# Optimization experiments

Measured on AMD Instinct MI355X. Metric: run time of the kernel, lower is better.

Reference implementation:

```python
import jax, jax.numpy as jnp
import numpy as np

EMBED_DIM = 1024
NUM_HEADS = 16
HEAD_DIM = EMBED_DIM // NUM_HEADS
B, S = 2, 2048
NEG = -1e20


def setup_inputs() -> dict:
    key = jax.random.key(0)
    ks = jax.random.split(key, 8)
    scale = 0.02
    return {
        "query": jax.random.normal(ks[0], (B, S, EMBED_DIM), jnp.float32),
        "keys": jax.random.normal(ks[1], (B, S, EMBED_DIM), jnp.float32),
        "values": jax.random.normal(ks[2], (B, S, EMBED_DIM), jnp.float32),
        "mask": jax.random.randint(ks[3], (1, 1, S, S), 0, 2, jnp.int32),
        "Wq": jax.random.normal(ks[4], (EMBED_DIM, EMBED_DIM), jnp.float32) * scale,
        "Wk": jax.random.normal(ks[5], (EMBED_DIM, EMBED_DIM), jnp.float32) * scale,
        "Wv": jax.random.normal(ks[6], (EMBED_DIM, EMBED_DIM), jnp.float32) * scale,
        "Wo": jax.random.normal(ks[7], (EMBED_DIM, EMBED_DIM), jnp.float32) * scale,
        "bo": jnp.zeros((EMBED_DIM,), jnp.float32),
    }


def reference(query, keys, values, mask, Wq, Wk, Wv, Wo, bo):
    N, Lq, _ = query.shape
    Lk = keys.shape[1]
    # torch nn.Linear: y = x @ W.T  (bias=False for Q/K/V)
    Q = (query @ Wq.T).reshape(N, Lq, NUM_HEADS, HEAD_DIM)
    K = (keys @ Wk.T).reshape(N, Lk, NUM_HEADS, HEAD_DIM)
    V = (values @ Wv.T).reshape(N, Lk, NUM_HEADS, HEAD_DIM)
    # NOTE: source scales by sqrt(embed_dim), not sqrt(head_dim) — kept faithful.
    energy = jnp.einsum("nqhd,nkhd->nhqk", Q, K) / jnp.sqrt(
        jnp.asarray(EMBED_DIM, Q.dtype)
    )
    energy = jnp.where(mask == 0, jnp.asarray(NEG, energy.dtype), energy)
    attention = jax.nn.softmax(energy, axis=3)
    out = jnp.einsum("nhqk,nkhd->nqhd", attention, V).reshape(N, Lq, EMBED_DIM)
    return out @ Wo.T + bo
```

## Files before the change

kernel.cpp:

```cpp
#include <hip/hip_runtime.h>
#include <stdint.h>

typedef __bf16 bf16;
typedef __bf16 bf16x4 __attribute__((ext_vector_type(4)));
typedef __bf16 bf16x8 __attribute__((ext_vector_type(8)));
typedef float f32x4 __attribute__((ext_vector_type(4)));
typedef float f32x16 __attribute__((ext_vector_type(16)));
typedef unsigned int uintx2 __attribute__((ext_vector_type(2)));
typedef unsigned int uintx4 __attribute__((ext_vector_type(4)));

#define MFMA16(a, b, c) __builtin_amdgcn_mfma_f32_16x16x32_bf16((a), (b), (c), 0, 0, 0)
#define MFMA32(a, b, c) __builtin_amdgcn_mfma_f32_32x32x16_bf16((a), (b), (c), 0, 0, 0)

__device__ __forceinline__ void gload16(const bf16* g, bf16* l) {
    __builtin_amdgcn_global_load_lds(
        (const __attribute__((address_space(1))) void*)g,
        (__attribute__((address_space(3))) void*)l, 16, 0, 0);
}

__device__ __forceinline__ float fast_exp2(float x) {
#if __has_builtin(__builtin_amdgcn_exp2f)
    return __builtin_amdgcn_exp2f(x);
#else
    return exp2f(x);
#endif
}

__global__ __launch_bounds__(256) void cvt_kernel(
    const float* __restrict__ q, const float* __restrict__ k, const float* __restrict__ v,
    const float* __restrict__ wq, const float* __restrict__ wk,
    const float* __restrict__ wv, const float* __restrict__ wo,
    const int* __restrict__ mask,
    bf16* __restrict__ qb, bf16* __restrict__ kb, bf16* __restrict__ vb,
    bf16* __restrict__ wqb, bf16* __restrict__ wkb, bf16* __restrict__ wvb,
    bf16* __restrict__ wob, unsigned long long* __restrict__ maskb)
{
    int z = blockIdx.z;
    if (z == 7) {
        int t16 = blockIdx.x * 256 + threadIdx.x;
        if (t16 >= 262144) return;
        const int4* mp = (const int4*)mask + (size_t)t16 * 4;
        unsigned bits = 0;
#pragma unroll
        for (int c = 0; c < 4; ++c) {
            int4 a = mp[c];
            bits |= (unsigned)(a.x != 0) << (c * 4 + 0);
            bits |= (unsigned)(a.y != 0) << (c * 4 + 1);
            bits |= (unsigned)(a.z != 0) << (c * 4 + 2);
            bits |= (unsigned)(a.w != 0) << (c * 4 + 3);
        }
        unsigned long long u = (unsigned long long)bits << (16 * (threadIdx.x & 3));
        u |= __shfl_xor(u, 1, 64);
        u |= __shfl_xor(u, 2, 64);
        if ((threadIdx.x & 3) == 0) maskb[t16 >> 2] = u;
        return;
    }
    const float* src; bf16* dst; int n;
    switch (z) {
        case 0:  src = q;  dst = qb;  n = 4194304; break;
        case 1:  src = k;  dst = kb;  n = 4194304; break;
        case 2:  src = v;  dst = vb;  n = 4194304; break;
        case 3:  src = wq; dst = wqb; n = 1048576; break;
        case 4:  src = wk; dst = wkb; n = 1048576; break;
        case 5:  src = wv; dst = wvb; n = 1048576; break;
        default: src = wo; dst = wob; n = 1048576; break;
    }
    int i = (blockIdx.x * 256 + threadIdx.x) * 8;
    if (i >= n) return;
    float4 f0 = *(const float4*)(src + i);
    float4 f1 = *(const float4*)(src + i + 4);
    bf16x8 o;
    o[0] = (bf16)f0.x; o[1] = (bf16)f0.y; o[2] = (bf16)f0.z; o[3] = (bf16)f0.w;
    o[4] = (bf16)f1.x; o[5] = (bf16)f1.y; o[6] = (bf16)f1.z; o[7] = (bf16)f1.w;
    *(bf16x8*)(dst + i) = o;
}

template <int OUTMODE>
__global__ __launch_bounds__(256) void gemm_kernel(
    const bf16* __restrict__ A0, const bf16* __restrict__ A1, const bf16* __restrict__ A2,
    const bf16* __restrict__ B0, const bf16* __restrict__ B1, const bf16* __restrict__ B2,
    bf16* __restrict__ C0, bf16* __restrict__ C1, bf16* __restrict__ Vt,
    const float* __restrict__ bias, float* __restrict__ outf)
{
    constexpr int TN    = (OUTMODE == 0) ? 128 : 64;
    constexpr int NI    = TN / 32;
    constexpr int BUFSZ = 4096 + TN * 32;
    __shared__ bf16 smem[3 * BUFSZ];

    const int f = blockIdx.x + 8 * blockIdx.y + ((OUTMODE == 0) ? 256 * blockIdx.z : 0);
    const int xcd = f & 7, sidx = f >> 3;
    const int z  = (OUTMODE == 0) ? (sidx >> 5) : 0;
    const int m0 = (xcd * 4 + (sidx & 3)) * 128;
    const int n0 = (OUTMODE == 0) ? ((sidx >> 2) & 7) * 128 : (sidx >> 2) * 64;

    const bf16* A = (z == 0) ? A0 : (z == 1) ? A1 : A2;
    const bf16* B = (z == 0) ? B0 : (z == 1) ? B1 : B2;

    const int tid  = threadIdx.x;
    const int lane = tid & 63;
    const int wave = tid >> 6;
    const int quad = lane >> 4;
    const int l16  = lane & 15;
    const int wm = (wave >> 1) * 64;
    const int wn = (wave & 1) * (TN / 2);

    const int lrow = lane >> 2;
    const int lcol = (lane & 3) * 8;

    f32x4 acc[4][NI] = {};

    const bf16* Ag = A + (size_t)(m0 + lrow) * 1024 + lcol;
    const bf16* Bg = B + (size_t)(n0 + lrow) * 1024 + lcol;

    bf16* buf0 = smem;
    bf16* buf1 = smem + BUFSZ;
    bf16* buf2 = smem + 2 * BUFSZ;

    auto stage = [&](bf16* base, int k0) {
#pragma unroll
        for (int j = 0; j < 2; ++j)
            gload16(Ag + (size_t)(wave * 32 + j * 16) * 1024 + k0,
                    base + (wave * 32 + j * 16) * 32);
        bf16* Btb = base + 4096;
        if constexpr (OUTMODE == 0) {
#pragma unroll
            for (int j = 0; j < 2; ++j)
                gload16(Bg + (size_t)(wave * 32 + j * 16) * 1024 + k0,
                        Btb + (wave * 32 + j * 16) * 32);
        } else {
            gload16(Bg + (size_t)(wave * 16) * 1024 + k0, Btb + (wave * 16) * 32);
        }
    };

    auto step = [&](bf16* cb, bf16* sb, int k0) {
        if (k0 == 992) {
            asm volatile("s_waitcnt vmcnt(0)" ::: "memory");
        } else if constexpr (OUTMODE == 0) {
            asm volatile("s_waitcnt vmcnt(4)" ::: "memory");
        } else {
            asm volatile("s_waitcnt vmcnt(3)" ::: "memory");
        }
        __builtin_amdgcn_s_barrier();
        __builtin_amdgcn_sched_barrier(0);
        if (k0 + 64 < 1024) stage(sb, k0 + 64);

        const bf16* Btb = cb + 4096;
        bf16x8 af[4], bg[NI];
#pragma unroll
        for (int i = 0; i < 4; ++i)
            af[i] = *(const bf16x8*)(cb + (wm + i * 16 + l16) * 32 + quad * 8);
#pragma unroll
        for (int j = 0; j < NI; ++j)
            bg[j] = *(const bf16x8*)(Btb + (wn + j * 16 + l16) * 32 + quad * 8);
#pragma unroll
        for (int i = 0; i < 4; ++i)
#pragma unroll
            for (int j = 0; j < NI; ++j)
                acc[i][j] = MFMA16(af[i], bg[j], acc[i][j]);
    };

    stage(buf0, 0);
    stage(buf1, 32);
    for (int k0 = 0; k0 < 960; k0 += 96) {
        step(buf0, buf2, k0);
        step(buf1, buf0, k0 + 32);
        step(buf2, buf1, k0 + 64);
    }
    step(buf0, buf2, 960);
    step(buf1, buf0, 992);

    if constexpr (OUTMODE == 0) {
        if (z == 2) {
            __syncthreads();
            const int qsw = ((quad & 1) << 1) | (quad >> 1);
#pragma unroll
            for (int i = 0; i < 4; ++i)
#pragma unroll
                for (int j = 0; j < 4; ++j) {
                    int e  = wn + j * 16 + l16;
                    int sp = wm + i * 16 + qsw * 4;
                    bf16x4 v4;
#pragma unroll
                    for (int r = 0; r < 4; ++r) v4[r] = (bf16)acc[i][j][r];
                    *(bf16x4*)(smem + e * 136 + sp) = v4;
                }
            __syncthreads();
            const int bq = m0 >> 11;
            const int srow = m0 & 2047;
#pragma unroll
            for (int c = 0; c < 2; ++c) {
                int idx = c * 256 + tid;
                int e = idx >> 2, sc = (idx & 3) * 32;
                bf16* dst = Vt + (size_t)(bq * 1024 + n0 + e) * 2048 + srow + sc;
#pragma unroll
                for (int kk = 0; kk < 4; ++kk)
                    *(bf16x8*)(dst + kk * 8) =
                        *(const bf16x8*)(smem + e * 136 + sc + kk * 8);
            }
            return;
        }
        bf16* C = (z == 0) ? C0 : C1;
        const float cs = (z == 0) ? 0.0450842200277800f : 1.0f;
#pragma unroll
        for (int i = 0; i < 4; ++i)
#pragma unroll
            for (int j = 0; j < 4; ++j) {
                int row = m0 + wm + i * 16 + quad * 4;
                int col = n0 + wn + j * 16 + l16;
#pragma unroll
                for (int r = 0; r < 4; ++r)
                    C[(row + r) * 1024 + col] = (bf16)(acc[i][j][r] * cs);
            }
    } else {
#pragma unroll
        for (int j = 0; j < NI; ++j) {
            int col = n0 + wn + j * 16 + l16;
            float bj = bias[col];
#pragma unroll
            for (int i = 0; i < 4; ++i) {
                int row = m0 + wm + i * 16 + quad * 4;
#pragma unroll
                for (int r = 0; r < 4; ++r)
                    outf[(row + r) * 1024 + col] = acc[i][j][r] + bj;
            }
        }
    }
}

__global__ __launch_bounds__(512, 4) void flash_kernel(
    const bf16* __restrict__ Q, const bf16* __restrict__ K, const bf16* __restrict__ Vt,
    const unsigned long long* __restrict__ maskb, bf16* __restrict__ O)
{
    __shared__ char smem[65536];

    const int tid  = threadIdx.x;
    const int lane = tid & 63;
    const int wave = tid >> 6;
    const int half = wave >> 2;
    const int w4   = wave & 3;
    const int l32  = lane & 31;
    const int hl   = lane >> 5;
    const int l7   = lane & 7;

    const int flat = blockIdx.x + 16 * (blockIdx.y + 16 * blockIdx.z);
    const int xcd  = flat & 7;
    const int slot = flat >> 3;
    const int bh   = xcd * 4 + (slot >> 4);
    const int h  = bh & 15;
    const int b  = bh >> 4;
    const int q0 = (slot & 15) * 128;
    const int qt = q0 + w4 * 32;

    bf16* hbase = (bf16*)smem + half * 16384;
    bf16* K0 = hbase;
    bf16* K1 = hbase + 4096;
    bf16* V0 = hbase + 8192;
    bf16* V1 = hbase + 12288;

    const bf16* Qb = Q + (size_t)(b * 2048 + qt + l32) * 1024 + h * 64 + hl * 8;
    bf16x8 qf[4];
#pragma unroll
    for (int ks = 0; ks < 4; ++ks) qf[ks] = *(const bf16x8*)(Qb + ks * 16);

    bf16x8 ones;
#pragma unroll
    for (int j = 0; j < 8; ++j) ones[j] = (bf16)1.0f;

    f32x16 acc[2] = {};
    f32x16 lacc = {};

    const int dmarow = lane >> 3;
    const int dmacol = (l7 ^ dmarow) * 8;
    const bf16* Kg = K + (size_t)(b * 2048 + w4 * 16 + dmarow) * 1024 + h * 64 + dmacol;
    const bf16* Vg = Vt + (size_t)((b * 16 + h) * 64 + w4 * 16 + dmarow) * 2048 + dmacol;
    const unsigned long long* Mg = maskb + (size_t)(qt + l32) * 32 + half * 16;
    const int kbase = half * 1024;

    auto stage = [&](bf16* Kd, bf16* Vd, int ktAbs) {
        gload16(Kg + (size_t)ktAbs * 1024,       Kd + (w4 * 16) * 64);
        gload16(Kg + (size_t)(ktAbs + 8) * 1024, Kd + (w4 * 16 + 8) * 64);
        gload16(Vg + ktAbs,                      Vd + (w4 * 16) * 64);
        gload16(Vg + ktAbs + 8 * 2048,           Vd + (w4 * 16 + 8) * 64);
    };

    unsigned long long mw = Mg[0];
    stage(K0, V0, kbase);

    auto body = [&](const bf16* Kc, const bf16* Vc, bf16* Kn, bf16* Vn, int it) {
        __syncthreads();
        unsigned long long mw_next = 0;
        if (it + 1 < 16) {
            stage(Kn, Vn, kbase + (it + 1) * 64);
            mw_next = Mg[it + 1];
        }

        bf16x8 pa[4];
#pragma unroll
        for (int t = 0; t < 2; ++t) {
            f32x16 s = {};
            __builtin_amdgcn_s_setprio(1);
#pragma unroll
            for (int ks = 0; ks < 4; ++ks) {
                bf16x8 ka = *(const bf16x8*)(Kc + (t * 32 + l32) * 64 +
                                             (((ks * 2 + hl) ^ l7) * 8));
                s = MFMA32(ka, qf[ks], s);
            }
            __builtin_amdgcn_s_setprio(0);
            unsigned mwt = (unsigned)(mw >> (t * 32 + 4 * hl));
            unsigned W[4][2];
#pragma unroll
            for (int g = 0; g < 4; ++g) {
                bf16x4 pv;
#pragma unroll
                for (int r = 0; r < 4; ++r) {
                    float ev = fast_exp2(s[g * 4 + r]);
                    unsigned msk = (unsigned)((int)(mwt << (31 - (8 * g + r))) >> 31);
                    unsigned evu = __builtin_bit_cast(unsigned, ev) & msk;
                    pv[r] = (bf16)__builtin_bit_cast(float, evu);
                }
                uintx2 u = __builtin_bit_cast(uintx2, pv);
                W[g][0] = u[0];
                W[g][1] = u[1];
            }
#pragma unroll
            for (int kh = 0; kh < 2; ++kh) {
                uintx4 aw = { W[2 * kh][0], W[2 * kh][1],
                              W[2 * kh + 1][0], W[2 * kh + 1][1] };
                pa[t * 2 + kh] = __builtin_bit_cast(bf16x8, aw);
            }
        }

        __builtin_amdgcn_s_setprio(1);
#pragma unroll
        for (int dt = 0; dt < 2; ++dt)
#pragma unroll
            for (int ks = 0; ks < 4; ++ks) {
                bf16x8 vb = *(const bf16x8*)(Vc + (dt * 32 + l32) * 64 +
                                             (((ks * 2 + hl) ^ l7) * 8));
                acc[dt] = MFMA32(pa[ks], vb, acc[dt]);
            }
#pragma unroll
        for (int ks = 0; ks < 4; ++ks)
            lacc = MFMA32(pa[ks], ones, lacc);
        __builtin_amdgcn_s_setprio(0);

        mw = mw_next;
    };

    for (int it = 0; it < 16; it += 2) {
        body(K0, V0, K1, V1, it);
        body(K1, V1, K0, V0, it + 1);
    }

    __syncthreads();
    float* cb = (float*)smem;
    float* ex = cb + (w4 * 64 + lane) * 4;
    if (half == 1) {
#pragma unroll
        for (int i = 0; i < 4; ++i) {
            f32x4 t0, t1, t2;
#pragma unroll
            for (int j = 0; j < 4; ++j) {
                t0[j] = acc[0][i * 4 + j];
                t1[j] = acc[1][i * 4 + j];
                t2[j] = lacc[i * 4 + j];
            }
            *(f32x4*)(ex + (i + 0) * 1024) = t0;
            *(f32x4*)(ex + (i + 4) * 1024) = t1;
            *(f32x4*)(ex + (i + 8) * 1024) = t2;
        }
    }
    __syncthreads();
    if (half == 0) {
#pragma unroll
        for (int i = 0; i < 4; ++i) {
            f32x4 t0 = *(const f32x4*)(ex + (i + 0) * 1024);
            f32x4 t1 = *(const f32x4*)(ex + (i + 4) * 1024);
            f32x4 t2 = *(const f32x4*)(ex + (i + 8) * 1024);
#pragma unroll
            for (int j = 0; j < 4; ++j) {
                acc[0][i * 4 + j] += t0[j];
                acc[1][i * 4 + j] += t1[j];
                lacc[i * 4 + j]   += t2[j];
            }
        }

        const size_t obase = (size_t)(b * 2048 + qt) * 1024 + h * 64;
#pragma unroll
        for (int g = 0; g < 4; ++g)
#pragma unroll
            for (int r = 0; r < 4; ++r) {
                int qr = 4 * hl + 8 * g + r;
                float inv = 1.0f / lacc[g * 4 + r];
                O[obase + (size_t)qr * 1024 + l32]      = (bf16)(acc[0][g * 4 + r] * inv);
                O[obase + (size_t)qr * 1024 + 32 + l32] = (bf16)(acc[1][g * 4 + r] * inv);
            }
    }
}

extern "C" void kernel_launch(void* const* d_in, const int* in_sizes, int n_in,
                              void* d_out, int out_size, void* d_ws, size_t ws_size,
                              hipStream_t stream)
{
    const float* q  = (const float*)d_in[0];
    const float* k  = (const float*)d_in[1];
    const float* v  = (const float*)d_in[2];
    const int* mask = (const int*)d_in[3];
    const float* wq = (const float*)d_in[4];
    const float* wk = (const float*)d_in[5];
    const float* wv = (const float*)d_in[6];
    const float* wo = (const float*)d_in[7];
    const float* bo = (const float*)d_in[8];
    float* out = (float*)d_out;

    char* p = (char*)d_ws;
    auto alloc = [&](size_t bytes) {
        char* r = p;
        p += (bytes + 255) & ~(size_t)255;
        return r;
    };
    const size_t SB = (size_t)4096 * 1024 * 2;
    const size_t WB = (size_t)1024 * 1024 * 2;
    bf16* qb  = (bf16*)alloc(SB);
    bf16* kb  = (bf16*)alloc(SB);
    bf16* vb  = (bf16*)alloc(SB);
    bf16* wqb = (bf16*)alloc(WB);
    bf16* wkb = (bf16*)alloc(WB);
    bf16* wvb = (bf16*)alloc(WB);
    bf16* wob = (bf16*)alloc(WB);
    bf16* Qp  = (bf16*)alloc(SB);
    bf16* Kp  = (bf16*)alloc(SB);
    bf16* Vtp = (bf16*)alloc(SB);
    bf16* Ob  = (bf16*)alloc(SB);
    unsigned long long* maskb = (unsigned long long*)alloc(2048 * 32 * 8);

    cvt_kernel<<<dim3(2048, 1, 8), 256, 0, stream>>>(
        q, k, v, wq, wk, wv, wo, mask, qb, kb, vb, wqb, wkb, wvb, wob, maskb);

    gemm_kernel<0><<<dim3(8, 32, 3), 256, 0, stream>>>(
        qb, kb, vb, wqb, wkb, wvb, Qp, Kp, Vtp, nullptr, nullptr);

    flash_kernel<<<dim3(16, 16, 2), 512, 0, stream>>>(Qp, Kp, Vtp, maskb, Ob);

    gemm_kernel<1><<<dim3(8, 64, 1), 256, 0, stream>>>(
        Ob, nullptr, nullptr, wob, nullptr, nullptr,
        nullptr, nullptr, nullptr, bo, out);
}
```

Measured before the change: 227.9 us.

## Fuse fp32-to-bf16 conversion of QKV inputs and weights into the projection GEMM

Removes the separate conversion pass over q/k/v and Wq/Wk/Wv. The QKV GEMM now loads fp32 tiles into registers, converts them to bf16, and writes them into a double-buffered LDS tile, using register prefetch in place of the direct global-to-LDS async loads. This avoids writing and re-reading roughly 30 MB of bf16 intermediates. The cost is twice the global read bytes per tile (fp32), repeated conversion work, and a simpler pipeline that may hide latency less well. The prep kernel now converts only Wo and packs the mask.

```diff
diff --git a/kernel.cpp b/kernel.cpp
--- a/kernel.cpp
+++ b/kernel.cpp
@@ -26,75 +26,57 @@
 #endif
 }
 
-__global__ __launch_bounds__(256) void cvt_kernel(
-    const float* __restrict__ q, const float* __restrict__ k, const float* __restrict__ v,
-    const float* __restrict__ wq, const float* __restrict__ wk,
-    const float* __restrict__ wv, const float* __restrict__ wo,
-    const int* __restrict__ mask,
-    bf16* __restrict__ qb, bf16* __restrict__ kb, bf16* __restrict__ vb,
-    bf16* __restrict__ wqb, bf16* __restrict__ wkb, bf16* __restrict__ wvb,
+__global__ __launch_bounds__(256) void prep_kernel(
+    const float* __restrict__ wo, const int* __restrict__ mask,
     bf16* __restrict__ wob, unsigned long long* __restrict__ maskb)
 {
-    int z = blockIdx.z;
-    if (z == 7) {
-        int t16 = blockIdx.x * 256 + threadIdx.x;
-        if (t16 >= 262144) return;
-        const int4* mp = (const int4*)mask + (size_t)t16 * 4;
-        unsigned bits = 0;
-#pragma unroll
-        for (int c = 0; c < 4; ++c) {
-            int4 a = mp[c];
-            bits |= (unsigned)(a.x != 0) << (c * 4 + 0);
-            bits |= (unsigned)(a.y != 0) << (c * 4 + 1);
-            bits |= (unsigned)(a.z != 0) << (c * 4 + 2);
-            bits |= (unsigned)(a.w != 0) << (c * 4 + 3);
-        }
-        unsigned long long u = (unsigned long long)bits << (16 * (threadIdx.x & 3));
-        u |= __shfl_xor(u, 1, 64);
-        u |= __shfl_xor(u, 2, 64);
-        if ((threadIdx.x & 3) == 0) maskb[t16 >> 2] = u;
+    int bid = blockIdx.x;
+    if (bid < 512) {
+        int i = (bid * 256 + threadIdx.x) * 8;
+        float4 f0 = *(const float4*)(wo + i);
+        float4 f1 = *(const float4*)(wo + i + 4);
+        bf16x8 o;
+        o[0] = (bf16)f0.x; o[1] = (bf16)f0.y; o[2] = (bf16)f0.z; o[3] = (bf16)f0.w;
+        o[4] = (bf16)f1.x; o[5] = (bf16)f1.y; o[6] = (bf16)f1.z; o[7] = (bf16)f1.w;
+        *(bf16x8*)(wob + i) = o;
         return;
     }
-    const float* src; bf16* dst; int n;
-    switch (z) {
-        case 0:  src = q;  dst = qb;  n = 4194304; break;
-        case 1:  src = k;  dst = kb;  n = 4194304; break;
-        case 2:  src = v;  dst = vb;  n = 4194304; break;
-        case 3:  src = wq; dst = wqb; n = 1048576; break;
-        case 4:  src = wk; dst = wkb; n = 1048576; break;
-        case 5:  src = wv; dst = wvb; n = 1048576; break;
-        default: src = wo; dst = wob; n = 1048576; break;
-    }
-    int i = (blockIdx.x * 256 + threadIdx.x) * 8;
-    if (i >= n) return;
-    float4 f0 = *(const float4*)(src + i);
-    float4 f1 = *(const float4*)(src + i + 4);
-    bf16x8 o;
-    o[0] = (bf16)f0.x; o[1] = (bf16)f0.y; o[2] = (bf16)f0.z; o[3] = (bf16)f0.w;
-    o[4] = (bf16)f1.x; o[5] = (bf16)f1.y; o[6] = (bf16)f1.z; o[7] = (bf16)f1.w;
-    *(bf16x8*)(dst + i) = o;
-}
-
-template <int OUTMODE>
-__global__ __launch_bounds__(256) void gemm_kernel(
-    const bf16* __restrict__ A0, const bf16* __restrict__ A1, const bf16* __restrict__ A2,
-    const bf16* __restrict__ B0, const bf16* __restrict__ B1, const bf16* __restrict__ B2,
-    bf16* __restrict__ C0, bf16* __restrict__ C1, bf16* __restrict__ Vt,
-    const float* __restrict__ bias, float* __restrict__ outf)
+    int t16 = (bid - 512) * 256 + threadIdx.x;
+    const int4* mp = (const int4*)mask + (size_t)t16 * 4;
+    unsigned bits = 0;
+#pragma unroll
+    for (int c = 0; c < 4; ++c) {
+        int4 a = mp[c];
+        bits |= (unsigned)(a.x != 0) << (c * 4 + 0);
+        bits |= (unsigned)(a.y != 0) << (c * 4 + 1);
+        bits |= (unsigned)(a.z != 0) << (c * 4 + 2);
+        bits |= (unsigned)(a.w != 0) << (c * 4 + 3);
+    }
+    unsigned long long u = (unsigned long long)bits << (16 * (threadIdx.x & 3));
+    u |= __shfl_xor(u, 1, 64);
+    u |= __shfl_xor(u, 2, 64);
+    if ((threadIdx.x & 3) == 0) maskb[t16 >> 2] = u;
+}
+
+__global__ __launch_bounds__(256) void gemm_qkv_kernel(
+    const float* __restrict__ A0, const float* __restrict__ A1, const float* __restrict__ A2,
+    const float* __restrict__ B0, const float* __restrict__ B1, const float* __restrict__ B2,
+    bf16* __restrict__ C0, bf16* __restrict__ C1, bf16* __restrict__ Vt)
 {
-    constexpr int TN    = (OUTMODE == 0) ? 128 : 64;
-    constexpr int NI    = TN / 32;
-    constexpr int BUFSZ = 4096 + TN * 32;
-    __shared__ bf16 smem[3 * BUFSZ];
-
-    const int f = blockIdx.x + 8 * blockIdx.y + ((OUTMODE == 0) ? 256 * blockIdx.z : 0);
+    __shared__ bf16 smem[17408];
+    bf16* A0l = smem;
+    bf16* B0l = smem + 4096;
+    bf16* A1l = smem + 8192;
+    bf16* B1l = smem + 12288;
+
+    const int f = blockIdx.x + 8 * blockIdx.y + 256 * blockIdx.z;
     const int xcd = f & 7, sidx = f >> 3;
-    const int z  = (OUTMODE == 0) ? (sidx >> 5) : 0;
+    const int z  = sidx >> 5;
     const int m0 = (xcd * 4 + (sidx & 3)) * 128;
-    const int n0 = (OUTMODE == 0) ? ((sidx >> 2) & 7) * 128 : (sidx >> 2) * 64;
-
-    const bf16* A = (z == 0) ? A0 : (z == 1) ? A1 : A2;
-    const bf16* B = (z == 0) ? B0 : (z == 1) ? B1 : B2;
+    const int n0 = ((sidx >> 2) & 7) * 128;
+
+    const float* A = (z == 0) ? A0 : (z == 1) ? A1 : A2;
+    const float* B = (z == 0) ? B0 : (z == 1) ? B1 : B2;
 
     const int tid  = threadIdx.x;
     const int lane = tid & 63;
@@ -102,15 +84,144 @@
     const int quad = lane >> 4;
     const int l16  = lane & 15;
     const int wm = (wave >> 1) * 64;
-    const int wn = (wave & 1) * (TN / 2);
+    const int wn = (wave & 1) * 64;
 
     const int lrow = lane >> 2;
     const int lcol = (lane & 3) * 8;
 
-    f32x4 acc[4][NI] = {};
-
-    const bf16* Ag = A + (size_t)(m0 + lrow) * 1024 + lcol;
-    const bf16* Bg = B + (size_t)(n0 + lrow) * 1024 + lcol;
+    f32x4 acc[4][4] = {};
+    float4 ra[2][2], rb[2][2];
+
+    const float* Ag = A + (size_t)(m0 + wave * 32 + lrow) * 1024 + lcol;
+    const float* Bg = B + (size_t)(n0 + wave * 32 + lrow) * 1024 + lcol;
+    const int lds_off = lrow * 32 + lcol;
+
+    auto loadregs = [&](int k0) {
+#pragma unroll
+        for (int j = 0; j < 2; ++j) {
+            ra[j][0] = *(const float4*)(Ag + (size_t)(j * 16) * 1024 + k0);
+            ra[j][1] = *(const float4*)(Ag + (size_t)(j * 16) * 1024 + k0 + 4);
+            rb[j][0] = *(const float4*)(Bg + (size_t)(j * 16) * 1024 + k0);
+            rb[j][1] = *(const float4*)(Bg + (size_t)(j * 16) * 1024 + k0 + 4);
+        }
+    };
+    auto writebufs = [&](bf16* At, bf16* Bt) {
+#pragma unroll
+        for (int j = 0; j < 2; ++j) {
+            bf16x8 oa, ob;
+            oa[0] = (bf16)ra[j][0].x; oa[1] = (bf16)ra[j][0].y;
+            oa[2] = (bf16)ra[j][0].z; oa[3] = (bf16)ra[j][0].w;
+            oa[4] = (bf16)ra[j][1].x; oa[5] = (bf16)ra[j][1].y;
+            oa[6] = (bf16)ra[j][1].z; oa[7] = (bf16)ra[j][1].w;
+            ob[0] = (bf16)rb[j][0].x; ob[1] = (bf16)rb[j][0].y;
+            ob[2] = (bf16)rb[j][0].z; ob[3] = (bf16)rb[j][0].w;
+            ob[4] = (bf16)rb[j][1].x; ob[5] = (bf16)rb[j][1].y;
+            ob[6] = (bf16)rb[j][1].z; ob[7] = (bf16)rb[j][1].w;
+            *(bf16x8*)(At + (wave * 32 + j * 16) * 32 + lds_off) = oa;
+            *(bf16x8*)(Bt + (wave * 32 + j * 16) * 32 + lds_off) = ob;
+        }
+    };
+    auto compute = [&](const bf16* At, const bf16* Bt) {
+        bf16x8 af[4], bg[4];
+#pragma unroll
+        for (int i = 0; i < 4; ++i)
+            af[i] = *(const bf16x8*)(At + (wm + i * 16 + l16) * 32 + quad * 8);
+#pragma unroll
+        for (int j = 0; j < 4; ++j)
+            bg[j] = *(const bf16x8*)(Bt + (wn + j * 16 + l16) * 32 + quad * 8);
+#pragma unroll
+        for (int i = 0; i < 4; ++i)
+#pragma unroll
+            for (int j = 0; j < 4; ++j)
+                acc[i][j] = MFMA16(af[i], bg[j], acc[i][j]);
+    };
+
+    loadregs(0);
+    writebufs(A0l, B0l);
+    loadregs(32);
+    for (int t = 0; t < 32; t += 2) {
+        __syncthreads();
+        writebufs(A1l, B1l);
+        if (t + 2 < 32) loadregs((t + 2) * 32);
+        compute(A0l, B0l);
+        __syncthreads();
+        if (t + 2 < 32) {
+            writebufs(A0l, B0l);
+            if (t + 3 < 32) loadregs((t + 3) * 32);
+        }
+        compute(A1l, B1l);
+    }
+
+    if (z == 2) {
+        __syncthreads();
+        const int qsw = ((quad & 1) << 1) | (quad >> 1);
+#pragma unroll
+        for (int i = 0; i < 4; ++i)
+#pragma unroll
+            for (int j = 0; j < 4; ++j) {
+                int e  = wn + j * 16 + l16;
+                int sp = wm + i * 16 + qsw * 4;
+                bf16x4 v4;
+#pragma unroll
+                for (int r = 0; r < 4; ++r) v4[r] = (bf16)acc[i][j][r];
+                *(bf16x4*)(smem + e * 136 + sp) = v4;
+            }
+        __syncthreads();
+        const int bq = m0 >> 11;
+        const int srow = m0 & 2047;
+#pragma unroll
+        for (int c = 0; c < 2; ++c) {
+            int idx = c * 256 + tid;
+            int e = idx >> 2, sc = (idx & 3) * 32;
+            bf16* dst = Vt + (size_t)(bq * 1024 + n0 + e) * 2048 + srow + sc;
+#pragma unroll
+            for (int kk = 0; kk < 4; ++kk)
+                *(bf16x8*)(dst + kk * 8) =
+                    *(const bf16x8*)(smem + e * 136 + sc + kk * 8);
+        }
+        return;
+    }
+    bf16* C = (z == 0) ? C0 : C1;
+    const float cs = (z == 0) ? 0.0450842200277800f : 1.0f;
+#pragma unroll
+    for (int i = 0; i < 4; ++i)
+#pragma unroll
+        for (int j = 0; j < 4; ++j) {
+            int row = m0 + wm + i * 16 + quad * 4;
+            int col = n0 + wn + j * 16 + l16;
+#pragma unroll
+            for (int r = 0; r < 4; ++r)
+                C[(row + r) * 1024 + col] = (bf16)(acc[i][j][r] * cs);
+        }
+}
+
+__global__ __launch_bounds__(256) void gemm_out_kernel(
+    const bf16* __restrict__ Ab, const bf16* __restrict__ Bb,
+    const float* __restrict__ bias, float* __restrict__ outf)
+{
+    constexpr int BUFSZ = 4096 + 2048;
+    __shared__ bf16 smem[3 * BUFSZ];
+
+    const int f = blockIdx.x + 8 * blockIdx.y;
+    const int xcd = f & 7, sidx = f >> 3;
+    const int m0 = (xcd * 4 + (sidx & 3)) * 128;
+    const int n0 = (sidx >> 2) * 64;
+
+    const int tid  = threadIdx.x;
+    const int lane = tid & 63;
+    const int wave = tid >> 6;
+    const int quad = lane >> 4;
+    const int l16  = lane & 15;
+    const int wm = (wave >> 1) * 64;
+    const int wn = (wave & 1) * 32;
+
+    const int lrow = lane >> 2;
+    const int lcol = (lane & 3) * 8;
+
+    f32x4 acc[4][2] = {};
+
+    const bf16* Ag = Ab + (size_t)(m0 + lrow) * 1024 + lcol;
+    const bf16* Bg = Bb + (size_t)(n0 + lrow) * 1024 + lcol;
 
     bf16* buf0 = smem;
     bf16* buf1 = smem + BUFSZ;
@@ -121,22 +232,12 @@
         for (int j = 0; j < 2; ++j)
             gload16(Ag + (size_t)(wave * 32 + j * 16) * 1024 + k0,
                     base + (wave * 32 + j * 16) * 32);
-        bf16* Btb = base + 4096;
-        if constexpr (OUTMODE == 0) {
-#pragma unroll
-            for (int j = 0; j < 2; ++j)
-                gload16(Bg + (size_t)(wave * 32 + j * 16) * 1024 + k0,
-                        Btb + (wave * 32 + j * 16) * 32);
-        } else {
-            gload16(Bg + (size_t)(wave * 16) * 1024 + k0, Btb + (wave * 16) * 32);
-        }
+        gload16(Bg + (size_t)(wave * 16) * 1024 + k0, base + 4096 + (wave * 16) * 32);
     };
 
     auto step = [&](bf16* cb, bf16* sb, int k0) {
         if (k0 == 992) {
             asm volatile("s_waitcnt vmcnt(0)" ::: "memory");
-        } else if constexpr (OUTMODE == 0) {
-            asm volatile("s_waitcnt vmcnt(4)" ::: "memory");
         } else {
             asm volatile("s_waitcnt vmcnt(3)" ::: "memory");
         }
@@ -145,17 +246,17 @@
         if (k0 + 64 < 1024) stage(sb, k0 + 64);
 
         const bf16* Btb = cb + 4096;
-        bf16x8 af[4], bg[NI];
+        bf16x8 af[4], bg[2];
 #pragma unroll
         for (int i = 0; i < 4; ++i)
             af[i] = *(const bf16x8*)(cb + (wm + i * 16 + l16) * 32 + quad * 8);
 #pragma unroll
-        for (int j = 0; j < NI; ++j)
+        for (int j = 0; j < 2; ++j)
             bg[j] = *(const bf16x8*)(Btb + (wn + j * 16 + l16) * 32 + quad * 8);
 #pragma unroll
         for (int i = 0; i < 4; ++i)
 #pragma unroll
-            for (int j = 0; j < NI; ++j)
+            for (int j = 0; j < 2; ++j)
                 acc[i][j] = MFMA16(af[i], bg[j], acc[i][j]);
     };
 
@@ -169,60 +270,16 @@
     step(buf0, buf2, 960);
     step(buf1, buf0, 992);
 
-    if constexpr (OUTMODE == 0) {
-        if (z == 2) {
-            __syncthreads();
-            const int qsw = ((quad & 1) << 1) | (quad >> 1);
-#pragma unroll
-            for (int i = 0; i < 4; ++i)
-#pragma unroll
-                for (int j = 0; j < 4; ++j) {
-                    int e  = wn + j * 16 + l16;
-                    int sp = wm + i * 16 + qsw * 4;
-                    bf16x4 v4;
-#pragma unroll
-                    for (int r = 0; r < 4; ++r) v4[r] = (bf16)acc[i][j][r];
-                    *(bf16x4*)(smem + e * 136 + sp) = v4;
-                }
-            __syncthreads();
-            const int bq = m0 >> 11;
-            const int srow = m0 & 2047;
-#pragma unroll
-            for (int c = 0; c < 2; ++c) {
-                int idx = c * 256 + tid;
-                int e = idx >> 2, sc = (idx & 3) * 32;
-                bf16* dst = Vt + (size_t)(bq * 1024 + n0 + e) * 2048 + srow + sc;
-#pragma unroll
-                for (int kk = 0; kk < 4; ++kk)
-                    *(bf16x8*)(dst + kk * 8) =
-                        *(const bf16x8*)(smem + e * 136 + sc + kk * 8);
-            }
-            return;
-        }
-        bf16* C = (z == 0) ? C0 : C1;
-        const float cs = (z == 0) ? 0.0450842200277800f : 1.0f;
-#pragma unroll
-        for (int i = 0; i < 4; ++i)
-#pragma unroll
-            for (int j = 0; j < 4; ++j) {
-                int row = m0 + wm + i * 16 + quad * 4;
-                int col = n0 + wn + j * 16 + l16;
-#pragma unroll
-                for (int r = 0; r < 4; ++r)
-                    C[(row + r) * 1024 + col] = (bf16)(acc[i][j][r] * cs);
-            }
-    } else {
-#pragma unroll
-        for (int j = 0; j < NI; ++j) {
-            int col = n0 + wn + j * 16 + l16;
-            float bj = bias[col];
-#pragma unroll
-            for (int i = 0; i < 4; ++i) {
-                int row = m0 + wm + i * 16 + quad * 4;
-#pragma unroll
-                for (int r = 0; r < 4; ++r)
-                    outf[(row + r) * 1024 + col] = acc[i][j][r] + bj;
-            }
+#pragma unroll
+    for (int j = 0; j < 2; ++j) {
+        int col = n0 + wn + j * 16 + l16;
+        float bj = bias[col];
+#pragma unroll
+        for (int i = 0; i < 4; ++i) {
+            int row = m0 + wm + i * 16 + quad * 4;
+#pragma unroll
+            for (int r = 0; r < 4; ++r)
+                outf[(row + r) * 1024 + col] = acc[i][j][r] + bj;
         }
     }
 }
@@ -421,12 +478,6 @@
     };
     const size_t SB = (size_t)4096 * 1024 * 2;
     const size_t WB = (size_t)1024 * 1024 * 2;
-    bf16* qb  = (bf16*)alloc(SB);
-    bf16* kb  = (bf16*)alloc(SB);
-    bf16* vb  = (bf16*)alloc(SB);
-    bf16* wqb = (bf16*)alloc(WB);
-    bf16* wkb = (bf16*)alloc(WB);
-    bf16* wvb = (bf16*)alloc(WB);
     bf16* wob = (bf16*)alloc(WB);
     bf16* Qp  = (bf16*)alloc(SB);
     bf16* Kp  = (bf16*)alloc(SB);
@@ -434,15 +485,12 @@
     bf16* Ob  = (bf16*)alloc(SB);
     unsigned long long* maskb = (unsigned long long*)alloc(2048 * 32 * 8);
 
-    cvt_kernel<<<dim3(2048, 1, 8), 256, 0, stream>>>(
-        q, k, v, wq, wk, wv, wo, mask, qb, kb, vb, wqb, wkb, wvb, wob, maskb);
-
-    gemm_kernel<0><<<dim3(8, 32, 3), 256, 0, stream>>>(
-        qb, kb, vb, wqb, wkb, wvb, Qp, Kp, Vtp, nullptr, nullptr);
+    prep_kernel<<<dim3(1536), 256, 0, stream>>>(wo, mask, wob, maskb);
+
+    gemm_qkv_kernel<<<dim3(8, 32, 3), 256, 0, stream>>>(
+        q, k, v, wq, wk, wv, Qp, Kp, Vtp);
 
     flash_kernel<<<dim3(16, 16, 2), 512, 0, stream>>>(Qp, Kp, Vtp, maskb, Ob);
 
-    gemm_kernel<1><<<dim3(8, 64, 1), 256, 0, stream>>>(
-        Ob, nullptr, nullptr, wob, nullptr, nullptr,
-        nullptr, nullptr, nullptr, bo, out);
-}
+    gemm_out_kernel<<<dim3(8, 64, 1), 256, 0, stream>>>(Ob, wob, bo, out);
+}
```

New measurement: 240.6 us. 5.6% more time.

## Split output projection K dimension across two wave groups with LDS reduction

Applied to the files above, without the earlier changes.

The output projection GEMM becomes its own kernel with 512 threads per block. Two groups of four waves each compute half of the K=1024 reduction in separate triple-buffered LDS regions, and their partial accumulators are summed through shared memory before the bias-added fp32 store. The goal is more waves per output tile, which should hide load latency better in a grid that is small relative to the CU count. The cost is an extra LDS exchange, two barriers, and higher LDS use per block.

```diff
diff --git a/kernel.cpp b/kernel.cpp
--- a/kernel.cpp
+++ b/kernel.cpp
@@ -75,23 +75,19 @@
     *(bf16x8*)(dst + i) = o;
 }
 
-template <int OUTMODE>
-__global__ __launch_bounds__(256) void gemm_kernel(
+__global__ __launch_bounds__(256) void gemm_qkv_kernel(
     const bf16* __restrict__ A0, const bf16* __restrict__ A1, const bf16* __restrict__ A2,
     const bf16* __restrict__ B0, const bf16* __restrict__ B1, const bf16* __restrict__ B2,
-    bf16* __restrict__ C0, bf16* __restrict__ C1, bf16* __restrict__ Vt,
-    const float* __restrict__ bias, float* __restrict__ outf)
+    bf16* __restrict__ C0, bf16* __restrict__ C1, bf16* __restrict__ Vt)
 {
-    constexpr int TN    = (OUTMODE == 0) ? 128 : 64;
-    constexpr int NI    = TN / 32;
-    constexpr int BUFSZ = 4096 + TN * 32;
+    constexpr int BUFSZ = 8192;
     __shared__ bf16 smem[3 * BUFSZ];
 
-    const int f = blockIdx.x + 8 * blockIdx.y + ((OUTMODE == 0) ? 256 * blockIdx.z : 0);
+    const int f = blockIdx.x + 8 * blockIdx.y + 256 * blockIdx.z;
     const int xcd = f & 7, sidx = f >> 3;
-    const int z  = (OUTMODE == 0) ? (sidx >> 5) : 0;
+    const int z  = sidx >> 5;
     const int m0 = (xcd * 4 + (sidx & 3)) * 128;
-    const int n0 = (OUTMODE == 0) ? ((sidx >> 2) & 7) * 128 : (sidx >> 2) * 64;
+    const int n0 = ((sidx >> 2) & 7) * 128;
 
     const bf16* A = (z == 0) ? A0 : (z == 1) ? A1 : A2;
     const bf16* B = (z == 0) ? B0 : (z == 1) ? B1 : B2;
@@ -102,12 +98,12 @@
     const int quad = lane >> 4;
     const int l16  = lane & 15;
     const int wm = (wave >> 1) * 64;
-    const int wn = (wave & 1) * (TN / 2);
+    const int wn = (wave & 1) * 64;
 
     const int lrow = lane >> 2;
     const int lcol = (lane & 3) * 8;
 
-    f32x4 acc[4][NI] = {};
+    f32x4 acc[4][4] = {};
 
     const bf16* Ag = A + (size_t)(m0 + lrow) * 1024 + lcol;
     const bf16* Bg = B + (size_t)(n0 + lrow) * 1024 + lcol;
@@ -122,40 +118,34 @@
             gload16(Ag + (size_t)(wave * 32 + j * 16) * 1024 + k0,
                     base + (wave * 32 + j * 16) * 32);
         bf16* Btb = base + 4096;
-        if constexpr (OUTMODE == 0) {
-#pragma unroll
-            for (int j = 0; j < 2; ++j)
-                gload16(Bg + (size_t)(wave * 32 + j * 16) * 1024 + k0,
-                        Btb + (wave * 32 + j * 16) * 32);
-        } else {
-            gload16(Bg + (size_t)(wave * 16) * 1024 + k0, Btb + (wave * 16) * 32);
-        }
+#pragma unroll
+        for (int j = 0; j < 2; ++j)
+            gload16(Bg + (size_t)(wave * 32 + j * 16) * 1024 + k0,
+                    Btb + (wave * 32 + j * 16) * 32);
     };
 
     auto step = [&](bf16* cb, bf16* sb, int k0) {
         if (k0 == 992) {
             asm volatile("s_waitcnt vmcnt(0)" ::: "memory");
-        } else if constexpr (OUTMODE == 0) {
+        } else {
             asm volatile("s_waitcnt vmcnt(4)" ::: "memory");
-        } else {
-            asm volatile("s_waitcnt vmcnt(3)" ::: "memory");
         }
         __builtin_amdgcn_s_barrier();
         __builtin_amdgcn_sched_barrier(0);
         if (k0 + 64 < 1024) stage(sb, k0 + 64);
 
         const bf16* Btb = cb + 4096;
-        bf16x8 af[4], bg[NI];
+        bf16x8 af[4], bg[4];
 #pragma unroll
         for (int i = 0; i < 4; ++i)
             af[i] = *(const bf16x8*)(cb + (wm + i * 16 + l16) * 32 + quad * 8);
 #pragma unroll
-        for (int j = 0; j < NI; ++j)
+        for (int j = 0; j < 4; ++j)
             bg[j] = *(const bf16x8*)(Btb + (wn + j * 16 + l16) * 32 + quad * 8);
 #pragma unroll
         for (int i = 0; i < 4; ++i)
 #pragma unroll
-            for (int j = 0; j < NI; ++j)
+            for (int j = 0; j < 4; ++j)
                 acc[i][j] = MFMA16(af[i], bg[j], acc[i][j]);
     };
 
@@ -169,51 +159,150 @@
     step(buf0, buf2, 960);
     step(buf1, buf0, 992);
 
-    if constexpr (OUTMODE == 0) {
-        if (z == 2) {
-            __syncthreads();
-            const int qsw = ((quad & 1) << 1) | (quad >> 1);
-#pragma unroll
-            for (int i = 0; i < 4; ++i)
-#pragma unroll
-                for (int j = 0; j < 4; ++j) {
-                    int e  = wn + j * 16 + l16;
-                    int sp = wm + i * 16 + qsw * 4;
-                    bf16x4 v4;
-#pragma unroll
-                    for (int r = 0; r < 4; ++r) v4[r] = (bf16)acc[i][j][r];
-                    *(bf16x4*)(smem + e * 136 + sp) = v4;
-                }
-            __syncthreads();
-            const int bq = m0 >> 11;
-            const int srow = m0 & 2047;
-#pragma unroll
-            for (int c = 0; c < 2; ++c) {
-                int idx = c * 256 + tid;
-                int e = idx >> 2, sc = (idx & 3) * 32;
-                bf16* dst = Vt + (size_t)(bq * 1024 + n0 + e) * 2048 + srow + sc;
-#pragma unroll
-                for (int kk = 0; kk < 4; ++kk)
-                    *(bf16x8*)(dst + kk * 8) =
-                        *(const bf16x8*)(smem + e * 136 + sc + kk * 8);
-            }
-            return;
-        }
-        bf16* C = (z == 0) ? C0 : C1;
-        const float cs = (z == 0) ? 0.0450842200277800f : 1.0f;
+    if (z == 2) {
+        __syncthreads();
+        const int qsw = ((quad & 1) << 1) | (quad >> 1);
 #pragma unroll
         for (int i = 0; i < 4; ++i)
 #pragma unroll
             for (int j = 0; j < 4; ++j) {
-                int row = m0 + wm + i * 16 + quad * 4;
-                int col = n0 + wn + j * 16 + l16;
-#pragma unroll
-                for (int r = 0; r < 4; ++r)
-                    C[(row + r) * 1024 + col] = (bf16)(acc[i][j][r] * cs);
-            }
-    } else {
-#pragma unroll
-        for (int j = 0; j < NI; ++j) {
+                int e  = wn + j * 16 + l16;
+                int sp = wm + i * 16 + qsw * 4;
+                bf16x4 v4;
+#pragma unroll
+                for (int r = 0; r < 4; ++r) v4[r] = (bf16)acc[i][j][r];
+                *(bf16x4*)(smem + e * 136 + sp) = v4;
+            }
+        __syncthreads();
+        const int bq = m0 >> 11;
+        const int srow = m0 & 2047;
+#pragma unroll
+        for (int c = 0; c < 2; ++c) {
+            int idx = c * 256 + tid;
+            int e = idx >> 2, sc = (idx & 3) * 32;
+            bf16* dst = Vt + (size_t)(bq * 1024 + n0 + e) * 2048 + srow + sc;
+#pragma unroll
+            for (int kk = 0; kk < 4; ++kk)
+                *(bf16x8*)(dst + kk * 8) =
+                    *(const bf16x8*)(smem + e * 136 + sc + kk * 8);
+        }
+        return;
+    }
+    bf16* C = (z == 0) ? C0 : C1;
+    const float cs = (z == 0) ? 0.0450842200277800f : 1.0f;
+#pragma unroll
+    for (int i = 0; i < 4; ++i)
+#pragma unroll
+        for (int j = 0; j < 4; ++j) {
+            int row = m0 + wm + i * 16 + quad * 4;
+            int col = n0 + wn + j * 16 + l16;
+#pragma unroll
+            for (int r = 0; r < 4; ++r)
+                C[(row + r) * 1024 + col] = (bf16)(acc[i][j][r] * cs);
+        }
+}
+
+__global__ __launch_bounds__(512) void gemm_out_kernel(
+    const bf16* __restrict__ Ab, const bf16* __restrict__ Bb,
+    const float* __restrict__ bias, float* __restrict__ outf)
+{
+    constexpr int BUFSZ = 4096 + 2048;
+    __shared__ bf16 smem[2 * 3 * BUFSZ];
+
+    const int f = blockIdx.x + 8 * blockIdx.y;
+    const int xcd = f & 7, sidx = f >> 3;
+    const int m0 = (xcd * 4 + (sidx & 3)) * 128;
+    const int n0 = (sidx >> 2) * 64;
+
+    const int tid  = threadIdx.x;
+    const int lane = tid & 63;
+    const int wave = tid >> 6;
+    const int half = wave >> 2;
+    const int w4   = wave & 3;
+    const int quad = lane >> 4;
+    const int l16  = lane & 15;
+    const int wm = (w4 >> 1) * 64;
+    const int wn = (w4 & 1) * 32;
+
+    const int lrow = lane >> 2;
+    const int lcol = (lane & 3) * 8;
+    const int kbase = half * 512;
+
+    f32x4 acc[4][2] = {};
+
+    const bf16* Ag = Ab + (size_t)(m0 + lrow) * 1024 + lcol + kbase;
+    const bf16* Bg = Bb + (size_t)(n0 + lrow) * 1024 + lcol + kbase;
+
+    bf16* hb   = smem + half * 3 * BUFSZ;
+    bf16* buf0 = hb;
+    bf16* buf1 = hb + BUFSZ;
+    bf16* buf2 = hb + 2 * BUFSZ;
+
+    auto stage = [&](bf16* base, int k0) {
+#pragma unroll
+        for (int j = 0; j < 2; ++j)
+            gload16(Ag + (size_t)(w4 * 32 + j * 16) * 1024 + k0,
+                    base + (w4 * 32 + j * 16) * 32);
+        gload16(Bg + (size_t)(w4 * 16) * 1024 + k0, base + 4096 + (w4 * 16) * 32);
+    };
+
+    auto step = [&](bf16* cb, bf16* sb, int k0) {
+        if (k0 == 480) {
+            asm volatile("s_waitcnt vmcnt(0)" ::: "memory");
+        } else {
+            asm volatile("s_waitcnt vmcnt(3)" ::: "memory");
+        }
+        __builtin_amdgcn_s_barrier();
+        __builtin_amdgcn_sched_barrier(0);
+        if (k0 + 64 < 512) stage(sb, k0 + 64);
+
+        const bf16* Btb = cb + 4096;
+        bf16x8 af[4], bg[2];
+#pragma unroll
+        for (int i = 0; i < 4; ++i)
+            af[i] = *(const bf16x8*)(cb + (wm + i * 16 + l16) * 32 + quad * 8);
+#pragma unroll
+        for (int j = 0; j < 2; ++j)
+            bg[j] = *(const bf16x8*)(Btb + (wn + j * 16 + l16) * 32 + quad * 8);
+#pragma unroll
+        for (int i = 0; i < 4; ++i)
+#pragma unroll
+            for (int j = 0; j < 2; ++j)
+                acc[i][j] = MFMA16(af[i], bg[j], acc[i][j]);
+    };
+
+    stage(buf0, 0);
+    stage(buf1, 32);
+    for (int k0 = 0; k0 < 480; k0 += 96) {
+        step(buf0, buf2, k0);
+        step(buf1, buf0, k0 + 32);
+        step(buf2, buf1, k0 + 64);
+    }
+    step(buf0, buf1, 480);
+
+    __syncthreads();
+    float* ex = (float*)smem + (w4 * 64 + lane) * 4;
+    if (half == 1) {
+#pragma unroll
+        for (int i = 0; i < 4; ++i) {
+            *(f32x4*)(ex + (i + 0) * 1024) = acc[i][0];
+            *(f32x4*)(ex + (i + 4) * 1024) = acc[i][1];
+        }
+    }
+    __syncthreads();
+    if (half == 0) {
+#pragma unroll
+        for (int i = 0; i < 4; ++i) {
+            f32x4 t0 = *(const f32x4*)(ex + (i + 0) * 1024);
+            f32x4 t1 = *(const f32x4*)(ex + (i + 4) * 1024);
+#pragma unroll
+            for (int j = 0; j < 4; ++j) {
+                acc[i][0][j] += t0[j];
+                acc[i][1][j] += t1[j];
+            }
+        }
+#pragma unroll
+        for (int j = 0; j < 2; ++j) {
             int col = n0 + wn + j * 16 + l16;
             float bj = bias[col];
 #pragma unroll
@@ -437,12 +526,10 @@
     cvt_kernel<<<dim3(2048, 1, 8), 256, 0, stream>>>(
         q, k, v, wq, wk, wv, wo, mask, qb, kb, vb, wqb, wkb, wvb, wob, maskb);
 
-    gemm_kernel<0><<<dim3(8, 32, 3), 256, 0, stream>>>(
-        qb, kb, vb, wqb, wkb, wvb, Qp, Kp, Vtp, nullptr, nullptr);
+    gemm_qkv_kernel<<<dim3(8, 32, 3), 256, 0, stream>>>(
+        qb, kb, vb, wqb, wkb, wvb, Qp, Kp, Vtp);
 
     flash_kernel<<<dim3(16, 16, 2), 512, 0, stream>>>(Qp, Kp, Vtp, maskb, Ob);
 
-    gemm_kernel<1><<<dim3(8, 64, 1), 256, 0, stream>>>(
-        Ob, nullptr, nullptr, wob, nullptr, nullptr,
-        nullptr, nullptr, nullptr, bo, out);
-}
+    gemm_out_kernel<<<dim3(8, 64), 512, 0, stream>>>(Ob, wob, bo, out);
+}
```

Result: no change. 226.5 us, median of 2 (-0.6%).
